# Kernel tuning notes

Hardware: AMD Instinct MI355X
Metric: run time of the kernel (lower is better)

Reference implementation:

```python
import jax, jax.numpy as jnp
import numpy as np

EPS = 1e-9
# exp factors for iterations i = 4,3,2,1,0,-1,-2 ; i == -2 -> 0.0
EXP_FACTORS = np.array([-(4.0 ** i) if i != -2 else 0.0 for i in range(4, -3, -1)], dtype=np.float32)


def setup_inputs() -> dict:
    key = jax.random.key(0)
    k1, k2 = jax.random.split(key)
    B, N, D = 16, 2048, 256
    preds = jax.random.normal(k1, (B, N, D), dtype=jnp.float32)
    labels = jax.random.normal(k2, (B, N, D), dtype=jnp.float32)
    return {"preds": preds, "labels": labels}


def _pairwise_dist(p1, p2):
    # [B,N,1] + [B,1,N] - 2 * p1 @ p2^T -> [B,N,N]
    p1_norm = jnp.sum(p1 * p1, axis=-1)[..., :, None]
    p2_norm = jnp.sum(p2 * p2, axis=-1)[..., None, :]
    return p1_norm + p2_norm - 2.0 * jnp.einsum('bnd,bmd->bnm', p1, p2)


def _approx_match(pwdist):
    B, N, _ = pwdist.shape
    match0 = jnp.zeros_like(pwdist)
    currency0 = jnp.ones((B, N, 1), dtype=pwdist.dtype)
    cost0 = jnp.ones((B, 1, N), dtype=pwdist.dtype)

    def body(carry, exp_factor):
        match, cost, currency = carry
        bids = jnp.exp(exp_factor * pwdist) * cost              # [B,N,N]
        bids = bids * currency / (jnp.sum(bids, axis=2, keepdims=True) + EPS)
        bid_wt = jnp.minimum(cost / (jnp.sum(bids, axis=1, keepdims=True) + EPS), 1.0)
        bids = bids * bid_wt
        match = match + bids
        cost = jnp.maximum(cost - jnp.sum(bids, axis=1, keepdims=True), 0.0)
        currency = jnp.maximum(currency - jnp.sum(bids, axis=2, keepdims=True), 0.0)
        return (match, cost, currency), None

    (match, _, _), _ = jax.lax.scan(body, (match0, cost0, currency0), jnp.asarray(EXP_FACTORS))
    return match


def reference(preds, labels):
    pwdist = _pairwise_dist(preds, labels)
    match = _approx_match(pwdist)
    return jnp.sum(match * pwdist)
```

## Files before the change

kernel.cpp:

```cpp
#include <hip/hip_runtime.h>
#include <cstdint>

#define B_ 16
#define N_ 2048
#define D_ 256
#define EPS_ 1e-9f

#define AS1 __attribute__((address_space(1)))
#define AS3 __attribute__((address_space(3)))

typedef float f4 __attribute__((ext_vector_type(4)));

__device__ float blockReduceSum(float x, float* red){
  int tid = threadIdx.x;
  red[tid] = x; __syncthreads();
  #pragma unroll
  for (int off = 128; off > 0; off >>= 1){
    if (tid < off) red[tid] += red[tid + off];
    __syncthreads();
  }
  float r = red[0]; __syncthreads();
  return r;
}

__global__ __launch_bounds__(256) void prep_kernel(
    const float* __restrict__ preds, const float* __restrict__ labels,
    unsigned char* __restrict__ pa8, unsigned char* __restrict__ pb8,
    float* __restrict__ pn, float* __restrict__ ln,
    float* __restrict__ cost, float* __restrict__ currency,
    int* __restrict__ dmin, float* __restrict__ Ppart,
    float* __restrict__ npart, float* __restrict__ out){
  int s = blockIdx.y;
  int tid = threadIdx.x;
  if (s == 0){
    int i = blockIdx.x * 256 + tid;
    if (i < B_ * N_){ cost[i] = 1.f; currency[i] = 1.f; }
    if (i < B_) dmin[i] = 0x7f7fffff;
    if (i == 0) out[0] = 0.f;
  }
  const float* src = s ? labels : preds;
  unsigned char* dst = s ? pb8 : pa8;
  float* norms = s ? ln : pn;
  int w = tid >> 6, lane = tid & 63;
  size_t row0 = (size_t)blockIdx.x * 16 + (size_t)w * 4;
  float4 v[4];
  #pragma unroll
  for (int q = 0; q < 4; q++)
    v[q] = ((const float4*)(src + (row0 + q) * D_))[lane];
  __shared__ f4 part[4][64];
  __shared__ float nred[4];
  f4 s4;
  s4[0] = v[0].x + v[1].x + v[2].x + v[3].x;
  s4[1] = v[0].y + v[1].y + v[2].y + v[3].y;
  s4[2] = v[0].z + v[1].z + v[2].z + v[3].z;
  s4[3] = v[0].w + v[1].w + v[2].w + v[3].w;
  float nsum = 0.f;
  #pragma unroll
  for (int q = 0; q < 4; q++){
    float sum = v[q].x*v[q].x + v[q].y*v[q].y + v[q].z*v[q].z + v[q].w*v[q].w;
    #pragma unroll
    for (int off = 32; off >= 1; off >>= 1) sum += __shfl_xor(sum, off);
    if (lane == 0){ norms[row0 + q] = sum; nsum += sum; }
    int pk = 0;
    pk = __builtin_amdgcn_cvt_pk_fp8_f32(v[q].x, v[q].y, pk, false);
    pk = __builtin_amdgcn_cvt_pk_fp8_f32(v[q].z, v[q].w, pk, true);
    ((unsigned int*)(dst + (row0 + q) * D_))[lane] = (unsigned int)pk;
  }
  part[w][lane] = s4;
  if (lane == 0) nred[w] = nsum;
  __syncthreads();
  if (tid < 64){
    f4 t = part[0][tid];
    #pragma unroll
    for (int q = 1; q < 4; q++){
      t[0] += part[q][tid][0]; t[1] += part[q][tid][1];
      t[2] += part[q][tid][2]; t[3] += part[q][tid][3];
    }
    *(f4*)(Ppart + ((size_t)s * 2048 + blockIdx.x) * 256 + tid * 4) = t;
  }
  if (tid == 0)
    npart[s * 2048 + blockIdx.x] = nred[0] + nred[1] + nred[2] + nred[3];
}

__global__ __launch_bounds__(512, 2) void gemm_minmax(
    const unsigned char* __restrict__ pa, const unsigned char* __restrict__ pbm,
    const float* __restrict__ pn, const float* __restrict__ ln,
    int* __restrict__ dmin)
{
  int lid = blockIdx.x;
  int l = lid >> 3;
  int b = 2 * (lid & 7) + (l >> 6);
  int t = l & 63;
  int tm = (t & 7) * 256, tn = (t >> 3) * 256;
  const unsigned char* A  = pa  + (size_t)b * N_ * D_;
  const unsigned char* Bm = pbm + (size_t)b * N_ * D_;
  __shared__ __align__(16) unsigned char As[2][256 * 128];
  __shared__ __align__(16) unsigned char Bs[2][256 * 128];
  __shared__ float minred[8];
  int tid = threadIdx.x, lane = tid & 63, w = tid >> 6;
  int wm = (w >> 2) * 128, wn = (w & 3) * 64;
  int quad = lane >> 4, l15 = lane & 15;

  f4 acc[8][4];
  #pragma unroll
  for (int i = 0; i < 8; i++)
    #pragma unroll
    for (int j = 0; j < 4; j++) acc[i][j] = (f4)0.f;

  int lr = lane >> 3, ch = lane & 7;
  int gch = (ch ^ lr) * 16;

  #pragma unroll
  for (int p = 0; p < 4; p++){
    int R = p * 64 + w * 8;
    int r = R + lr;
    __builtin_amdgcn_global_load_lds(
        (const AS1 unsigned int*)(const void*)&A[(size_t)(tm + r) * D_ + gch],
        (AS3 unsigned int*)(void*)&As[0][R * 128], 16, 0, 0);
    __builtin_amdgcn_global_load_lds(
        (const AS1 unsigned int*)(const void*)&Bm[(size_t)(tn + r) * D_ + gch],
        (AS3 unsigned int*)(void*)&Bs[0][R * 128], 16, 0, 0);
  }

  int buf = 0;
  for (int ki = 0; ki < 2; ki++){
    __syncthreads();
    if (ki < 1){
      int kt = 128;
      #pragma unroll
      for (int p = 0; p < 4; p++){
        int R = p * 64 + w * 8;
        int r = R + lr;
        __builtin_amdgcn_global_load_lds(
            (const AS1 unsigned int*)(const void*)&A[(size_t)(tm + r) * D_ + kt + gch],
            (AS3 unsigned int*)(void*)&As[buf ^ 1][R * 128], 16, 0, 0);
        __builtin_amdgcn_global_load_lds(
            (const AS1 unsigned int*)(const void*)&Bm[(size_t)(tn + r) * D_ + kt + gch],
            (AS3 unsigned int*)(void*)&Bs[buf ^ 1][R * 128], 16, 0, 0);
      }
    }
    #pragma unroll
    for (int s = 0; s < 4; s++){
      long af[8], bf[4];
      int base = s * 2 + (quad >> 1);
      int sub = (quad & 1) * 8;
      #pragma unroll
      for (int i = 0; i < 8; i++){
        int ra = wm + i * 16 + l15;
        af[i] = *(const long*)(&As[buf][ra * 128 + ((base ^ (ra & 7)) * 16) + sub]);
      }
      #pragma unroll
      for (int jj = 0; jj < 4; jj++){
        int rb = wn + jj * 16 + l15;
        bf[jj] = *(const long*)(&Bs[buf][rb * 128 + ((base ^ (rb & 7)) * 16) + sub]);
      }
      #pragma unroll
      for (int i = 0; i < 8; i++)
        #pragma unroll
        for (int jj = 0; jj < 4; jj++)
          acc[i][jj] = __builtin_amdgcn_mfma_f32_16x16x32_fp8_fp8(af[i], bf[jj], acc[i][jj], 0, 0, 0);
    }
    buf ^= 1;
  }

  float4 pnr[8];
  float lnr[4];
  #pragma unroll
  for (int i = 0; i < 8; i++)
    pnr[i] = *(const float4*)&pn[(size_t)b * N_ + tm + wm + i * 16 + quad * 4];
  #pragma unroll
  for (int jj = 0; jj < 4; jj++)
    lnr[jj] = ln[(size_t)b * N_ + tn + wn + jj * 16 + l15];

  float mind = 3.4e38f;
  #pragma unroll
  for (int i = 0; i < 8; i++){
    float pv[4] = {pnr[i].x, pnr[i].y, pnr[i].z, pnr[i].w};
    #pragma unroll
    for (int jj = 0; jj < 4; jj++){
      #pragma unroll
      for (int reg = 0; reg < 4; reg++){
        float v = pv[reg] + lnr[jj] - 2.f * acc[i][jj][reg];
        mind = fminf(mind, v);
      }
    }
  }
  #pragma unroll
  for (int off = 32; off >= 1; off >>= 1) mind = fminf(mind, __shfl_xor(mind, off));
  if (lane == 0) minred[w] = mind;
  __syncthreads();
  if (tid == 0){
    float m = minred[0];
    #pragma unroll
    for (int q = 1; q < 8; q++) m = fminf(m, minred[q]);
    atomicMin(&dmin[b], __float_as_int(fmaxf(m, 0.f)));
  }
}

__global__ __launch_bounds__(256) void tail(
    const float* __restrict__ preds, const float* __restrict__ labels,
    const float* __restrict__ pn, const float* __restrict__ ln,
    float* __restrict__ cost, float* __restrict__ currency,
    const int* __restrict__ dmin, const float* __restrict__ Ppart,
    const float* __restrict__ npart, float* __restrict__ out)
{
  const float EF[6] = {-256.f, -64.f, -16.f, -4.f, -1.f, -0.25f};
  int b = blockIdx.x, tid = threadIdx.x;
  float dm = __int_as_float(dmin[b]);
  __shared__ float red[256];

  if (-0.25f * (dm - 16.f) < -55.f){
    float Pc = 0.f, Lc = 0.f;
    for (int k = 0; k < 128; k++){
      Pc += Ppart[((size_t)b * 128 + k) * 256 + tid];
      Lc += Ppart[((size_t)(2048 + b * 128 + k)) * 256 + tid];
    }
    float np = (tid < 128) ? npart[b * 128 + tid] : 0.f;
    float nl = (tid < 128) ? npart[2048 + b * 128 + tid] : 0.f;
    float Spn = blockReduceSum(np, red);
    float Sln = blockReduceSum(nl, red);
    float dot = blockReduceSum(Pc * Lc, red);
    if (tid == 0) atomicAdd(out, Spn + Sln - dot * (1.f / 1024.f));
    return;
  }

  __shared__ float alpha_l[N_];
  __shared__ float prow[D_];
  const float* A  = preds  + (size_t)b * N_ * D_;
  const float* Bm = labels + (size_t)b * N_ * D_;
  const float* pnb = pn + (size_t)b * N_;
  const float* lnb = ln + (size_t)b * N_;
  float* costb = cost + (size_t)b * N_;
  float* curb  = currency + (size_t)b * N_;
  for (int it = 0; it < 6; it++){
    float ef = EF[it];
    if (ef * (dm - 16.f) < -55.f) continue;
    float cost_c[8], colsum_c[8], bw_c[8], costnew_c[8];
    #pragma unroll
    for (int j = 0; j < 8; j++){ cost_c[j] = costb[j*256+tid]; colsum_c[j] = 0.f; }
    for (int r = 0; r < N_; r++){
      prow[tid] = A[(size_t)r * D_ + tid];
      __syncthreads();
      float s_c[8], rs = 0.f;
      for (int j = 0; j < 8; j++){
        int m = j*256+tid; float dot = 0.f;
        for (int k = 0; k < D_; k++) dot += prow[k] * Bm[(size_t)m * D_ + k];
        float d = pnb[r] + lnb[m] - 2.f*dot;
        float s = __expf(ef * d) * cost_c[j];
        s_c[j] = s; rs += s;
      }
      float tot = blockReduceSum(rs, red);
      float a = curb[r] / (tot + EPS_);
      if (tid == 0) alpha_l[r] = a;
      #pragma unroll
      for (int j = 0; j < 8; j++) colsum_c[j] += s_c[j] * a;
      __syncthreads();
    }
    #pragma unroll
    for (int j = 0; j < 8; j++){
      float cs = colsum_c[j];
      float bw = fminf(cost_c[j] / (cs + EPS_), 1.f);
      bw_c[j] = bw; costnew_c[j] = fmaxf(cost_c[j] - bw*cs, 0.f);
    }
    float contrib = 0.f;
    for (int r = 0; r < N_; r++){
      prow[tid] = A[(size_t)r * D_ + tid];
      __syncthreads();
      float a = alpha_l[r], rbs = 0.f;
      for (int j = 0; j < 8; j++){
        int m = j*256+tid; float dot = 0.f;
        for (int k = 0; k < D_; k++) dot += prow[k] * Bm[(size_t)m * D_ + k];
        float d = pnb[r] + lnb[m] - 2.f*dot;
        float bid = __expf(ef * d) * cost_c[j] * a * bw_c[j];
        rbs += bid; contrib += bid * d;
      }
      float tot = blockReduceSum(rbs, red);
      if (tid == 0) curb[r] = fmaxf(curb[r] - tot, 0.f);
      __syncthreads();
    }
    #pragma unroll
    for (int j = 0; j < 8; j++) costb[j*256+tid] = costnew_c[j];
    float ctot = blockReduceSum(contrib, red);
    if (tid == 0) atomicAdd(out, ctot);
    __syncthreads();
  }
  float s = 0.f;
  #pragma unroll
  for (int j = 0; j < 8; j++) s += costb[j*256+tid];
  float Sc = blockReduceSum(s, red);
  float sa = 0.f, spn = 0.f;
  #pragma unroll
  for (int j = 0; j < 8; j++){
    int i = j*256+tid;
    float a = curb[i] / (Sc + EPS_);
    alpha_l[i] = a; sa += a; spn += a * pnb[i];
  }
  float Sa  = blockReduceSum(sa, red);
  float Spn = blockReduceSum(spn, red);
  float Pc = 0.f;
  for (int r = 0; r < N_; r++)
    Pc += alpha_l[r] * A[(size_t)r * D_ + tid];
  __syncthreads();
  float sv = 0.f, sln = 0.f;
  #pragma unroll
  for (int j = 0; j < 8; j++){
    int i = j*256+tid;
    float c = costb[i];
    float bw = fminf(c / (c * Sa + EPS_), 1.f);
    float vv = c * bw;
    alpha_l[i] = vv; sv += vv; sln += vv * lnb[i];
  }
  float Sv  = blockReduceSum(sv, red);
  float Sln = blockReduceSum(sln, red);
  float Lc = 0.f;
  for (int m = 0; m < N_; m++)
    Lc += alpha_l[m] * Bm[(size_t)m * D_ + tid];
  float dot = blockReduceSum(Pc * Lc, red);
  if (tid == 0) atomicAdd(out, Spn * Sv + Sa * Sln - 2.f * dot);
}

extern "C" void kernel_launch(void* const* d_in, const int* in_sizes, int n_in,
                              void* d_out, int out_size, void* d_ws, size_t ws_size,
                              hipStream_t stream)
{
  const float* preds  = (const float*)d_in[0];
  const float* labels = (const float*)d_in[1];
  float* out = (float*)d_out;
  char* ws = (char*)d_ws;
  const size_t BN = (size_t)B_ * N_;
  size_t off = 0;
  float* cost     = (float*)(ws + off); off += BN * 4;
  float* currency = (float*)(ws + off); off += BN * 4;
  float* pn       = (float*)(ws + off); off += BN * 4;
  float* ln       = (float*)(ws + off); off += BN * 4;
  int*   dmin     = (int*)(ws + off);   off += 256;
  float* npart    = (float*)(ws + off); off += (size_t)2 * 2048 * 4;
  float* Ppart    = (float*)(ws + off); off += (size_t)2 * 2048 * 256 * 4;
  unsigned char* pa8 = (unsigned char*)(ws + off); off += BN * D_;
  unsigned char* pb8 = (unsigned char*)(ws + off); off += BN * D_;

  prep_kernel<<<dim3((unsigned)(BN / 16), 2), 256, 0, stream>>>(
      preds, labels, pa8, pb8, pn, ln, cost, currency, dmin, Ppart, npart, out);
  gemm_minmax<<<dim3(1024), 512, 0, stream>>>(pa8, pb8, pn, ln, dmin);
  tail<<<dim3(B_), 256, 0, stream>>>(preds, labels, pn, ln, cost, currency, dmin,
                                     Ppart, npart, out);
}
```

Measured before the change: 140.6 us.

## Make gemm_minmax blocks persistent over four M tiles with resident B tile

Each block now keeps a full 256x256 B tile resident in LDS and loops over four consecutive 256-row A tiles. It reduces each tile's min on the fly and resets the accumulators. The grid shrinks from 1024 to 256 blocks, so B loads and block launch overhead drop. In exchange there are fewer blocks than CUs, and LDS per block grows, which may lower occupancy and parallelism.

Measured after the change: 136.9 us. 1.03x faster.

```diff
diff --git a/kernel.cpp b/kernel.cpp
--- a/kernel.cpp
+++ b/kernel.cpp
@@ -88,57 +88,70 @@
     int* __restrict__ dmin)
 {
   int lid = blockIdx.x;
+  int xcd = lid & 7;
   int l = lid >> 3;
-  int b = 2 * (lid & 7) + (l >> 6);
-  int t = l & 63;
-  int tm = (t & 7) * 256, tn = (t >> 3) * 256;
+  int b = 2 * xcd + (l >> 4);
+  int p = l & 15;
+  int tn = (p & 7) * 256;
+  int tmb = (p >> 3) * 1024;
   const unsigned char* A  = pa  + (size_t)b * N_ * D_;
   const unsigned char* Bm = pbm + (size_t)b * N_ * D_;
+  __shared__ __align__(16) unsigned char Bs[256 * 256];
   __shared__ __align__(16) unsigned char As[2][256 * 128];
-  __shared__ __align__(16) unsigned char Bs[2][256 * 128];
   __shared__ float minred[8];
   int tid = threadIdx.x, lane = tid & 63, w = tid >> 6;
   int wm = (w >> 2) * 128, wn = (w & 3) * 64;
   int quad = lane >> 4, l15 = lane & 15;
 
-  f4 acc[8][4];
-  #pragma unroll
-  for (int i = 0; i < 8; i++)
-    #pragma unroll
-    for (int j = 0; j < 4; j++) acc[i][j] = (f4)0.f;
-
+  {
+    int rB = lane >> 4;
+    int c  = lane & 15;
+    #pragma unroll
+    for (int q = 0; q < 8; q++){
+      int R = q * 32 + w * 4;
+      int r = R + rB;
+      int gc = c ^ (r & 7);
+      __builtin_amdgcn_global_load_lds(
+          (const AS1 unsigned int*)(const void*)&Bm[(size_t)(tn + r) * D_ + gc * 16],
+          (AS3 unsigned int*)(void*)&Bs[R * 256 + lane * 16], 16, 0, 0);
+    }
+  }
   int lr = lane >> 3, ch = lane & 7;
   int gch = (ch ^ lr) * 16;
-
-  #pragma unroll
-  for (int p = 0; p < 4; p++){
-    int R = p * 64 + w * 8;
-    int r = R + lr;
+  #pragma unroll
+  for (int pq = 0; pq < 4; pq++){
+    int R = pq * 64 + w * 8;
     __builtin_amdgcn_global_load_lds(
-        (const AS1 unsigned int*)(const void*)&A[(size_t)(tm + r) * D_ + gch],
+        (const AS1 unsigned int*)(const void*)&A[(size_t)(tmb + R + lr) * D_ + gch],
         (AS3 unsigned int*)(void*)&As[0][R * 128], 16, 0, 0);
-    __builtin_amdgcn_global_load_lds(
-        (const AS1 unsigned int*)(const void*)&Bm[(size_t)(tn + r) * D_ + gch],
-        (AS3 unsigned int*)(void*)&Bs[0][R * 128], 16, 0, 0);
-  }
+  }
+
+  f4 acc[8][4];
+  #pragma unroll
+  for (int i = 0; i < 8; i++)
+    #pragma unroll
+    for (int j = 0; j < 4; j++) acc[i][j] = (f4)0.f;
+
+  float mind = 3.4e38f;
+  float lnr[4];
+  #pragma unroll
+  for (int jj = 0; jj < 4; jj++)
+    lnr[jj] = ln[(size_t)b * N_ + tn + wn + jj * 16 + l15];
 
   int buf = 0;
-  for (int ki = 0; ki < 2; ki++){
+  for (int step = 0; step < 8; step++){
     __syncthreads();
-    if (ki < 1){
-      int kt = 128;
-      #pragma unroll
-      for (int p = 0; p < 4; p++){
-        int R = p * 64 + w * 8;
-        int r = R + lr;
+    if (step < 7){
+      int t1 = (step + 1) >> 1, k1 = (step + 1) & 1;
+      #pragma unroll
+      for (int pq = 0; pq < 4; pq++){
+        int R = pq * 64 + w * 8;
         __builtin_amdgcn_global_load_lds(
-            (const AS1 unsigned int*)(const void*)&A[(size_t)(tm + r) * D_ + kt + gch],
+            (const AS1 unsigned int*)(const void*)&A[(size_t)(tmb + t1 * 256 + R + lr) * D_ + k1 * 128 + gch],
             (AS3 unsigned int*)(void*)&As[buf ^ 1][R * 128], 16, 0, 0);
-        __builtin_amdgcn_global_load_lds(
-            (const AS1 unsigned int*)(const void*)&Bm[(size_t)(tn + r) * D_ + kt + gch],
-            (AS3 unsigned int*)(void*)&Bs[buf ^ 1][R * 128], 16, 0, 0);
-      }
-    }
+      }
+    }
+    int ki = step & 1;
     #pragma unroll
     for (int s = 0; s < 4; s++){
       long af[8], bf[4];
@@ -149,10 +162,11 @@
         int ra = wm + i * 16 + l15;
         af[i] = *(const long*)(&As[buf][ra * 128 + ((base ^ (ra & 7)) * 16) + sub]);
       }
+      int gB = ki * 8 + base;
       #pragma unroll
       for (int jj = 0; jj < 4; jj++){
         int rb = wn + jj * 16 + l15;
-        bf[jj] = *(const long*)(&Bs[buf][rb * 128 + ((base ^ (rb & 7)) * 16) + sub]);
+        bf[jj] = *(const long*)(&Bs[rb * 256 + ((gB ^ (rb & 7)) * 16) + sub]);
       }
       #pragma unroll
       for (int i = 0; i < 8; i++)
@@ -160,31 +174,30 @@
         for (int jj = 0; jj < 4; jj++)
           acc[i][jj] = __builtin_amdgcn_mfma_f32_16x16x32_fp8_fp8(af[i], bf[jj], acc[i][jj], 0, 0, 0);
     }
+    if (ki == 1){
+      int t = step >> 1;
+      int tm = tmb + t * 256;
+      float4 pnr[8];
+      #pragma unroll
+      for (int i = 0; i < 8; i++)
+        pnr[i] = *(const float4*)&pn[(size_t)b * N_ + tm + wm + i * 16 + quad * 4];
+      #pragma unroll
+      for (int i = 0; i < 8; i++){
+        float pv[4] = {pnr[i].x, pnr[i].y, pnr[i].z, pnr[i].w};
+        #pragma unroll
+        for (int jj = 0; jj < 4; jj++){
+          #pragma unroll
+          for (int reg = 0; reg < 4; reg++){
+            float v = pv[reg] + lnr[jj] - 2.f * acc[i][jj][reg];
+            mind = fminf(mind, v);
+            acc[i][jj][reg] = 0.f;
+          }
+        }
+      }
+    }
     buf ^= 1;
   }
 
-  float4 pnr[8];
-  float lnr[4];
-  #pragma unroll
-  for (int i = 0; i < 8; i++)
-    pnr[i] = *(const float4*)&pn[(size_t)b * N_ + tm + wm + i * 16 + quad * 4];
-  #pragma unroll
-  for (int jj = 0; jj < 4; jj++)
-    lnr[jj] = ln[(size_t)b * N_ + tn + wn + jj * 16 + l15];
-
-  float mind = 3.4e38f;
-  #pragma unroll
-  for (int i = 0; i < 8; i++){
-    float pv[4] = {pnr[i].x, pnr[i].y, pnr[i].z, pnr[i].w};
-    #pragma unroll
-    for (int jj = 0; jj < 4; jj++){
-      #pragma unroll
-      for (int reg = 0; reg < 4; reg++){
-        float v = pv[reg] + lnr[jj] - 2.f * acc[i][jj][reg];
-        mind = fminf(mind, v);
-      }
-    }
-  }
   #pragma unroll
   for (int off = 32; off >= 1; off >>= 1) mind = fminf(mind, __shfl_xor(mind, off));
   if (lane == 0) minred[w] = mind;
@@ -341,7 +354,7 @@
 
   prep_kernel<<<dim3((unsigned)(BN / 16), 2), 256, 0, stream>>>(
       preds, labels, pa8, pb8, pn, ln, cost, currency, dmin, Ppart, npart, out);
-  gemm_minmax<<<dim3(1024), 512, 0, stream>>>(pa8, pb8, pn, ln, dmin);
+  gemm_minmax<<<dim3(256), 512, 0, stream>>>(pa8, pb8, pn, ln, dmin);
   tail<<<dim3(B_), 256, 0, stream>>>(preds, labels, pn, ln, cost, currency, dmin,
                                      Ppart, npart, out);
 }
```
